# Kernel tuning notes

Measured on AMD Instinct MI355X. Metric: run time of the kernel, lower is better.

Reference implementation:

```python
import jax, jax.numpy as jnp
import numpy as np

B, S, H, D = 2, 2048, 16, 64


def setup_inputs() -> dict:
    key = jax.random.key(0)
    kq, kk, kv, km = jax.random.split(key, 4)
    q = jax.random.normal(kq, (B, S, H, D), dtype=jnp.float32)
    k = jax.random.normal(kk, (B, S, H, D), dtype=jnp.float32)
    v = jax.random.normal(kv, (B, S, H, D), dtype=jnp.float32)
    pattern_mask = jax.random.bernoulli(km, 0.1, (S, S))
    return {"q": q, "k": k, "v": v, "pattern_mask": pattern_mask}


def reference(q, k, v, pattern_mask):
    # Faithful math of the torch module: for each query row i, attend only to
    # columns j where pattern_mask[i, j]; softmax over the selected columns
    # per (batch, head); rows with no selected columns produce zeros.
    head_dim = q.shape[-1]
    scale = 1.0 / jnp.sqrt(jnp.asarray(head_dim, dtype=q.dtype))
    # scores: [B, H, S_q, S_k]
    scores = jnp.einsum('bihd,bjhd->bhij', q, k) * scale
    neg = jnp.finfo(scores.dtype).min
    masked = jnp.where(pattern_mask[None, None, :, :], scores, neg)
    attn = jax.nn.softmax(masked, axis=-1)
    # zero out rows with no active columns (softmax over all-masked row is uniform garbage)
    row_has = jnp.any(pattern_mask, axis=-1)  # [S]
    attn = jnp.where(row_has[None, None, :, None], attn, jnp.zeros((), dtype=attn.dtype))
    # output: [B, S, H, D]
    out = jnp.einsum('bhij,bjhd->bihd', attn, v)
    return out
```

## Files before the change

### kernel.cpp

```cpp
#include <hip/hip_runtime.h>
#include <hip/hip_bf16.h>
#include <math.h>

#define SLEN 2048
#define NBATCH 2
#define NH 16
#define DH 64
#define WPR 64
#define NROUND 32
#define TILEB 16384
#define CONVBLK (NBATCH * NH * NROUND)
#define PACKBLK (SLEN * WPR / 256)

typedef __attribute__((ext_vector_type(4))) short short4v;
typedef __attribute__((ext_vector_type(8))) short short8v;
typedef __attribute__((ext_vector_type(4))) float float4v;
typedef __attribute__((ext_vector_type(16))) float float16v;

__device__ __forceinline__ unsigned short f2bf(float f) {
  unsigned u = __float_as_uint(f);
  u += 0x7fffu + ((u >> 16) & 1u);
  return (unsigned short)(u >> 16);
}

__device__ __forceinline__ float fexp2(float x) {
#if __has_builtin(__builtin_amdgcn_exp2f)
  return __builtin_amdgcn_exp2f(x);
#else
  return __expf(x * 0.6931471805599453f);
#endif
}

__device__ __forceinline__ unsigned pack_bf2(float a, float b) {
  unsigned ua = __float_as_uint(a); ua += 0x7fffu + ((ua >> 16) & 1u);
  unsigned ub = __float_as_uint(b); ub += 0x7fffu + ((ub >> 16) & 1u);
  return __builtin_amdgcn_perm(ub, ua, 0x07060302u);
}

__device__ __forceinline__ unsigned cvtpk(float lo, float hi) {
  unsigned r;
  asm("v_cvt_pk_bf16_f32 %0, %1, %2" : "=v"(r) : "v"(lo), "v"(hi));
  return r;
}

__device__ __forceinline__ unsigned nib4(unsigned w) {
  return ((w * 0x01020408u) >> 24) & 0xFu;
}

__global__ __launch_bounds__(256) void prep_kernel(
    const float* __restrict__ kk, const float* __restrict__ vv,
    const void* __restrict__ mask,
    char* __restrict__ img, unsigned* __restrict__ packed) {
  const int tid = threadIdx.x;
  if (blockIdx.x >= CONVBLK) {
    const int w = (blockIdx.x - CONVBLK) * 256 + tid;
    const uint4* bp = (const uint4*)((const char*)mask + (size_t)w * 32);
    uint4 x = bp[0], y = bp[1];
    const unsigned orw = (x.x | x.y) | (x.z | x.w) | (y.x | y.y) | (y.z | y.w);
    __shared__ int s0, sm;
    if (tid == 0) { s0 = 0; sm = 0; }
    __syncthreads();
    const int lane0 = ((tid & 63) == 0);
    if (__any((orw & 0x000000ffu) != 0) && lane0) atomicOr(&s0, 1);
    if (__any((orw & 0xffffff00u) != 0) && lane0) atomicOr(&sm, 1);
    __syncthreads();
    unsigned bits;
    if (s0 && sm) {
      bits = nib4(x.x) | (nib4(x.y) << 4) | (nib4(x.z) << 8) | (nib4(x.w) << 12) |
             (nib4(y.x) << 16) | (nib4(y.y) << 20) | (nib4(y.z) << 24) | (nib4(y.w) << 28);
    } else {
      const unsigned* m = (const unsigned*)mask + (size_t)w * 32;
      bits = 0u;
#pragma unroll
      for (int j = 0; j < 32; j++) bits |= (m[j] ? 1u : 0u) << j;
    }
    packed[w] = bits;
    return;
  }
  const int bid = blockIdx.x;
  const int t = bid & 31;
  const int bh = bid >> 5;
  const int b = bh >> 4, h = bh & 15;
  char* timg = img + (size_t)bid * TILEB;

  {
    const int r = tid >> 2;
    const int dg = (tid & 3) << 4;
    const float* src = kk + (((size_t)(b * SLEN + t * 64 + r) * NH + h) * DH + dg);
    const int f = ((r >> 5) << 2) + (dg >> 4);
    char* base = timg + f * 1024 + (r & 31) * 16;
    float4v x0 = *(const float4v*)(src);
    float4v x1 = *(const float4v*)(src + 4);
    float4v x2 = *(const float4v*)(src + 8);
    float4v x3 = *(const float4v*)(src + 12);
    union { unsigned u[4]; short8v s8; } lo, hi;
    lo.u[0] = pack_bf2(x0.x, x0.y); lo.u[1] = pack_bf2(x0.z, x0.w);
    lo.u[2] = pack_bf2(x1.x, x1.y); lo.u[3] = pack_bf2(x1.z, x1.w);
    hi.u[0] = pack_bf2(x2.x, x2.y); hi.u[1] = pack_bf2(x2.z, x2.w);
    hi.u[2] = pack_bf2(x3.x, x3.y); hi.u[3] = pack_bf2(x3.z, x3.w);
    *(short8v*)(base) = lo.s8;
    *(short8v*)(base + 512) = hi.s8;
  }
  {
    const int d = tid >> 2;
    const int kg = (tid & 3) << 4;
    const float* src = vv + ((size_t)(b * SLEN + t * 64 + kg) * NH + h) * DH + d;
    const int fbase = 8 + ((d >> 5) << 2);
    const int l31d = d & 31;
#pragma unroll
    for (int i = 0; i < 16; i++) {
      const int p = kg + i;
      float x = src[(size_t)i * (NH * DH)];
      const int f = fbase + 2 * (p >> 5) + ((p >> 4) & 1);
      const int lane = ((p >> 2) & 1) * 32 + l31d;
      const int slot = 4 * ((p >> 3) & 1) + (p & 3);
      *(unsigned short*)(timg + f * 1024 + lane * 16 + slot * 2) = f2bf(x);
    }
  }
}

__global__ __launch_bounds__(256, 2) void sattn_fast8(
    const float* __restrict__ q, const unsigned* __restrict__ pmask,
    const char* __restrict__ img, float* __restrict__ out) {
  const int tid = threadIdx.x;
  const int xcd = blockIdx.x & 7;
  const int j = blockIdx.x >> 3;
  const int bh = xcd * 4 + (j >> 4);
  const int chunk = j & 15;
  const int b = bh >> 4;
  const int hd = bh & 15;
  const int wave = tid >> 6;
  const int lane = tid & 63;
  const int l31 = lane & 31;
  const int hl = lane >> 5;

  const int qrow = chunk * 128 + wave * 32 + l31;
  const int qw = qrow * WPR;

  const float SCL2 = 0.18033688011112042f;
  short8v qf[4];
  {
    const float* qp = q + (((size_t)b * SLEN + qrow) * NH + hd) * DH;
#pragma unroll
    for (int ds = 0; ds < 4; ds++) {
      float4v x0 = *(const float4v*)(qp + ds * 16 + hl * 8);
      float4v x1 = *(const float4v*)(qp + ds * 16 + hl * 8 + 4);
      union { unsigned u[4]; short8v s8; } cv;
      cv.u[0] = pack_bf2(x0.x * SCL2, x0.y * SCL2);
      cv.u[1] = pack_bf2(x0.z * SCL2, x0.w * SCL2);
      cv.u[2] = pack_bf2(x1.x * SCL2, x1.y * SCL2);
      cv.u[3] = pack_bf2(x1.z * SCL2, x1.w * SCL2);
      qf[ds] = cv.s8;
    }
  }

  const char* pt = img + (size_t)bh * (NROUND * TILEB) + lane * 16;

  float16v acc0 = {}, acc1 = {};
  float lsum = 0.f;

  short8v kf0 = *(const short8v*)(pt + 0 * 1024);
  short8v kf1 = *(const short8v*)(pt + 1 * 1024);
  short8v kf2 = *(const short8v*)(pt + 2 * 1024);
  short8v kf3 = *(const short8v*)(pt + 3 * 1024);
  short8v kf4 = *(const short8v*)(pt + 4 * 1024);
  short8v kf5 = *(const short8v*)(pt + 5 * 1024);
  short8v kf6 = *(const short8v*)(pt + 6 * 1024);
  short8v kf7 = *(const short8v*)(pt + 7 * 1024);
  short8v vf0 = *(const short8v*)(pt + 8 * 1024);
  short8v vf1 = *(const short8v*)(pt + 9 * 1024);
  short8v vf2 = *(const short8v*)(pt + 10 * 1024);
  short8v vf3 = *(const short8v*)(pt + 11 * 1024);
  short8v vf4 = *(const short8v*)(pt + 12 * 1024);
  short8v vf5 = *(const short8v*)(pt + 13 * 1024);
  short8v vf6 = *(const short8v*)(pt + 14 * 1024);
  short8v vf7 = *(const short8v*)(pt + 15 * 1024);
  uint2 m = *(const uint2*)&pmask[qw];

  for (int t = 0; t < NROUND; t++) {
    const unsigned m0 = m.x, m1 = m.y;
    const int tn = (t + 1 < NROUND) ? t + 1 : t;
    const char* pn = pt + (size_t)tn * TILEB;

    __builtin_amdgcn_s_setprio(1);
    float16v st0 = {}, st1 = {};
    st0 = __builtin_amdgcn_mfma_f32_32x32x16_bf16(kf0, qf[0], st0, 0, 0, 0);
    st1 = __builtin_amdgcn_mfma_f32_32x32x16_bf16(kf4, qf[0], st1, 0, 0, 0);
    st0 = __builtin_amdgcn_mfma_f32_32x32x16_bf16(kf1, qf[1], st0, 0, 0, 0);
    st1 = __builtin_amdgcn_mfma_f32_32x32x16_bf16(kf5, qf[1], st1, 0, 0, 0);
    st0 = __builtin_amdgcn_mfma_f32_32x32x16_bf16(kf2, qf[2], st0, 0, 0, 0);
    st1 = __builtin_amdgcn_mfma_f32_32x32x16_bf16(kf6, qf[2], st1, 0, 0, 0);
    st0 = __builtin_amdgcn_mfma_f32_32x32x16_bf16(kf3, qf[3], st0, 0, 0, 0);
    st1 = __builtin_amdgcn_mfma_f32_32x32x16_bf16(kf7, qf[3], st1, 0, 0, 0);
    __builtin_amdgcn_s_setprio(0);

    kf0 = *(const short8v*)(pn + 0 * 1024);
    kf1 = *(const short8v*)(pn + 1 * 1024);
    kf2 = *(const short8v*)(pn + 2 * 1024);
    kf3 = *(const short8v*)(pn + 3 * 1024);
    kf4 = *(const short8v*)(pn + 4 * 1024);
    kf5 = *(const short8v*)(pn + 5 * 1024);
    kf6 = *(const short8v*)(pn + 6 * 1024);
    kf7 = *(const short8v*)(pn + 7 * 1024);
    m = *(const uint2*)&pmask[qw + 2 * tn];

    float p0[16], p1[16];
#pragma unroll
    for (int u = 0; u < 4; u++) {
      const unsigned hw0 = m0 >> (8 * u + 4 * hl);
      const unsigned hw1 = m1 >> (8 * u + 4 * hl);
      {
        float a0 = fexp2(st0[4 * u + 0]); a0 = (hw0 & 1u) ? a0 : 0.f;
        float a1 = fexp2(st0[4 * u + 1]); a1 = (hw0 & 2u) ? a1 : 0.f;
        float a2 = fexp2(st0[4 * u + 2]); a2 = (hw0 & 4u) ? a2 : 0.f;
        float a3 = fexp2(st0[4 * u + 3]); a3 = (hw0 & 8u) ? a3 : 0.f;
        lsum += (a0 + a1) + (a2 + a3);
        p0[4 * u + 0] = a0; p0[4 * u + 1] = a1; p0[4 * u + 2] = a2; p0[4 * u + 3] = a3;
      }
      {
        float a0 = fexp2(st1[4 * u + 0]); a0 = (hw1 & 1u) ? a0 : 0.f;
        float a1 = fexp2(st1[4 * u + 1]); a1 = (hw1 & 2u) ? a1 : 0.f;
        float a2 = fexp2(st1[4 * u + 2]); a2 = (hw1 & 4u) ? a2 : 0.f;
        float a3 = fexp2(st1[4 * u + 3]); a3 = (hw1 & 8u) ? a3 : 0.f;
        lsum += (a0 + a1) + (a2 + a3);
        p1[4 * u + 0] = a0; p1[4 * u + 1] = a1; p1[4 * u + 2] = a2; p1[4 * u + 3] = a3;
      }
    }
    short8v pf0, pf1, pf2, pf3;
    {
      union { unsigned u[4]; short8v s8; } c0, c1, c2, c3;
#pragma unroll
      for (int jj = 0; jj < 4; jj++) {
        c0.u[jj] = cvtpk(p0[2 * jj], p0[2 * jj + 1]);
        c1.u[jj] = cvtpk(p0[8 + 2 * jj], p0[8 + 2 * jj + 1]);
        c2.u[jj] = cvtpk(p1[2 * jj], p1[2 * jj + 1]);
        c3.u[jj] = cvtpk(p1[8 + 2 * jj], p1[8 + 2 * jj + 1]);
      }
      pf0 = c0.s8; pf1 = c1.s8; pf2 = c2.s8; pf3 = c3.s8;
    }

    __builtin_amdgcn_s_setprio(1);
    acc0 = __builtin_amdgcn_mfma_f32_32x32x16_bf16(vf0, pf0, acc0, 0, 0, 0);
    acc1 = __builtin_amdgcn_mfma_f32_32x32x16_bf16(vf4, pf0, acc1, 0, 0, 0);
    acc0 = __builtin_amdgcn_mfma_f32_32x32x16_bf16(vf1, pf1, acc0, 0, 0, 0);
    acc1 = __builtin_amdgcn_mfma_f32_32x32x16_bf16(vf5, pf1, acc1, 0, 0, 0);
    acc0 = __builtin_amdgcn_mfma_f32_32x32x16_bf16(vf2, pf2, acc0, 0, 0, 0);
    acc1 = __builtin_amdgcn_mfma_f32_32x32x16_bf16(vf6, pf2, acc1, 0, 0, 0);
    acc0 = __builtin_amdgcn_mfma_f32_32x32x16_bf16(vf3, pf3, acc0, 0, 0, 0);
    acc1 = __builtin_amdgcn_mfma_f32_32x32x16_bf16(vf7, pf3, acc1, 0, 0, 0);
    __builtin_amdgcn_s_setprio(0);

    vf0 = *(const short8v*)(pn + 8 * 1024);
    vf1 = *(const short8v*)(pn + 9 * 1024);
    vf2 = *(const short8v*)(pn + 10 * 1024);
    vf3 = *(const short8v*)(pn + 11 * 1024);
    vf4 = *(const short8v*)(pn + 12 * 1024);
    vf5 = *(const short8v*)(pn + 13 * 1024);
    vf6 = *(const short8v*)(pn + 14 * 1024);
    vf7 = *(const short8v*)(pn + 15 * 1024);
  }

  lsum += __shfl_xor(lsum, 32);
  const float inv = (lsum > 0.f) ? 1.f / lsum : 0.f;
  float* op = out + (((size_t)b * SLEN + qrow) * NH + hd) * DH;
#pragma unroll
  for (int u = 0; u < 4; u++) {
    float4v o0, o1;
    o0.x = acc0[4 * u + 0] * inv; o0.y = acc0[4 * u + 1] * inv;
    o0.z = acc0[4 * u + 2] * inv; o0.w = acc0[4 * u + 3] * inv;
    o1.x = acc1[4 * u + 0] * inv; o1.y = acc1[4 * u + 1] * inv;
    o1.z = acc1[4 * u + 2] * inv; o1.w = acc1[4 * u + 3] * inv;
    *(float4v*)(op + 8 * u + 4 * hl) = o0;
    *(float4v*)(op + 32 + 8 * u + 4 * hl) = o1;
  }
}

__global__ __launch_bounds__(256) void sattn_fallback(
    const float* __restrict__ q, const float* __restrict__ kk,
    const float* __restrict__ vv, const unsigned int* __restrict__ pmask,
    float* __restrict__ out) {
  __shared__ __align__(16) unsigned short Kt[16 * 64];
  __shared__ __align__(16) unsigned short Vt[64 * 20];

  const int tid = threadIdx.x;
  const int chunk = blockIdx.x & 31;
  const int bh = blockIdx.x >> 5;
  const int b = bh >> 4;
  const int h = bh & 15;
  const int wave = tid >> 6;
  const int lane = tid & 63;
  const int lq = lane & 15;
  const int g = lane >> 4;

  const int qrow = chunk * 64 + wave * 16 + lq;

  short4v qf[4];
  {
    const float* qp = q + (((size_t)b * SLEN + qrow) * NH + h) * DH;
#pragma unroll
    for (int ks = 0; ks < 4; ks++) {
      float4v x = *(const float4v*)(qp + ks * 16 + g * 4);
      short4v s;
      s.x = (short)f2bf(x.x); s.y = (short)f2bf(x.y);
      s.z = (short)f2bf(x.z); s.w = (short)f2bf(x.w);
      qf[ks] = s;
    }
  }

  const int srow = tid >> 4;
  const int scol = (tid & 15) * 4;
  const size_t kvbase = (size_t)b * SLEN * (NH * DH) + (size_t)h * DH;

  float4v acc[4] = {};
  float m_run = -INFINITY;
  float l_run = 0.f;

  for (int t = 0; t < SLEN / 16; t++) {
    const int kbase = t * 16;
    __syncthreads();
    {
      const size_t rowoff = kvbase + (size_t)(kbase + srow) * (NH * DH) + scol;
      float4v x = *(const float4v*)(kk + rowoff);
      short4v s;
      s.x = (short)f2bf(x.x); s.y = (short)f2bf(x.y);
      s.z = (short)f2bf(x.z); s.w = (short)f2bf(x.w);
      const int off = (scol * 2) ^ ((srow & 7) << 4);
      *(short4v*)((char*)Kt + srow * 128 + off) = s;

      float4v y = *(const float4v*)(vv + rowoff);
      Vt[(scol + 0) * 20 + srow] = f2bf(y.x);
      Vt[(scol + 1) * 20 + srow] = f2bf(y.y);
      Vt[(scol + 2) * 20 + srow] = f2bf(y.z);
      Vt[(scol + 3) * 20 + srow] = f2bf(y.w);
    }
    __syncthreads();

    float4v stv = {0.f, 0.f, 0.f, 0.f};
#pragma unroll
    for (int ks = 0; ks < 4; ks++) {
      const int off = ((ks * 16 + g * 4) * 2) ^ ((lq & 7) << 4);
      short4v kf = *(const short4v*)((const char*)Kt + lq * 128 + off);
      stv = __builtin_amdgcn_mfma_f32_16x16x16bf16_1k(kf, qf[ks], stv, 0, 0, 0);
    }

    const unsigned int mw = pmask[qrow * WPR + (kbase >> 5)];
    const int shift = (kbase & 16) + g * 4;
    float sc[4];
    float tmax = -INFINITY;
#pragma unroll
    for (int r = 0; r < 4; r++) {
      bool a = (mw >> (shift + r)) & 1u;
      sc[r] = a ? stv[r] * 0.125f : -INFINITY;
      tmax = fmaxf(tmax, sc[r]);
    }
    tmax = fmaxf(tmax, __shfl_xor(tmax, 16));
    tmax = fmaxf(tmax, __shfl_xor(tmax, 32));
    const float mnew = fmaxf(m_run, tmax);
    const float muse = (mnew > -1e37f) ? mnew : 0.f;
    const float alpha = __expf(m_run - muse);
    float p[4], tsum = 0.f;
#pragma unroll
    for (int r = 0; r < 4; r++) {
      p[r] = __expf(sc[r] - muse);
      tsum += p[r];
    }
    tsum += __shfl_xor(tsum, 16);
    tsum += __shfl_xor(tsum, 32);
    l_run = l_run * alpha + tsum;
    m_run = mnew;

    short4v pfv;
    pfv.x = (short)f2bf(p[0]); pfv.y = (short)f2bf(p[1]);
    pfv.z = (short)f2bf(p[2]); pfv.w = (short)f2bf(p[3]);

#pragma unroll
    for (int n = 0; n < 4; n++) {
      acc[n][0] *= alpha; acc[n][1] *= alpha;
      acc[n][2] *= alpha; acc[n][3] *= alpha;
      short4v vf = *(const short4v*)((const char*)Vt + ((n * 16 + lq) * 20 + g * 4) * 2);
      acc[n] = __builtin_amdgcn_mfma_f32_16x16x16bf16_1k(vf, pfv, acc[n], 0, 0, 0);
    }
  }

  const float inv = (l_run > 0.f) ? 1.f / l_run : 0.f;
  float* op = out + (((size_t)b * SLEN + qrow) * NH + h) * DH;
#pragma unroll
  for (int n = 0; n < 4; n++) {
    float4v o;
    o.x = acc[n][0] * inv; o.y = acc[n][1] * inv;
    o.z = acc[n][2] * inv; o.w = acc[n][3] * inv;
    *(float4v*)(op + n * 16 + g * 4) = o;
  }
}

extern "C" void kernel_launch(void* const* d_in, const int* in_sizes, int n_in,
                              void* d_out, int out_size, void* d_ws, size_t ws_size,
                              hipStream_t stream) {
  const float* q = (const float*)d_in[0];
  const float* k = (const float*)d_in[1];
  const float* v = (const float*)d_in[2];
  const void* mask = d_in[3];
  float* out = (float*)d_out;

  unsigned int* packed = (unsigned int*)((char*)d_ws + 256);
  char* img = (char*)d_ws + (1 << 20);
  const size_t need = (size_t)(1 << 20) + (size_t)CONVBLK * TILEB;

  prep_kernel<<<CONVBLK + PACKBLK, 256, 0, stream>>>(k, v, mask, img, packed);
  if (ws_size >= need) {
    sattn_fast8<<<NBATCH * NH * (SLEN / 128), 256, 0, stream>>>(q, packed, img, out);
  } else {
    sattn_fallback<<<NBATCH * NH * (SLEN / 64), 256, 0, stream>>>(q, k, v, packed, out);
  }
}
```

Before: 69.59 us.

## Split key range across wave pairs with LDS reduction to double block count

Each block now covers 64 query rows instead of 128. The four waves form two pairs, and each pair processes half of the 32 key tiles. The partial accumulators and row sums from the second half are combined through shared memory before the final normalization and store. The grid doubles and the launch bound allows 4 blocks per CU, which raises parallelism and shortens each wave's serial loop, at the cost of a shared-memory reduction, a block barrier, and more register pressure under the tighter occupancy target.

```diff
diff --git a/kernel.cpp b/kernel.cpp
--- a/kernel.cpp
+++ b/kernel.cpp
@@ -119,23 +119,27 @@
   }
 }
 
-__global__ __launch_bounds__(256, 2) void sattn_fast8(
+__global__ __launch_bounds__(256, 4) void sattn_fast9(
     const float* __restrict__ q, const unsigned* __restrict__ pmask,
     const char* __restrict__ img, float* __restrict__ out) {
+  __shared__ float red[2][64][33];
+
   const int tid = threadIdx.x;
   const int xcd = blockIdx.x & 7;
   const int j = blockIdx.x >> 3;
-  const int bh = xcd * 4 + (j >> 4);
-  const int chunk = j & 15;
+  const int bh = xcd * 4 + (j >> 5);
+  const int chunk = j & 31;
   const int b = bh >> 4;
   const int hd = bh & 15;
   const int wave = tid >> 6;
   const int lane = tid & 63;
   const int l31 = lane & 31;
   const int hl = lane >> 5;
-
-  const int qrow = chunk * 128 + wave * 32 + l31;
-  const int qw = qrow * WPR;
+  const int qsub = wave & 1;
+  const int khalf = wave >> 1;
+
+  const int qrow = chunk * 64 + qsub * 32 + l31;
+  const int qw = qrow * WPR + 2 * (khalf * 16);
 
   const float SCL2 = 0.18033688011112042f;
   short8v qf[4];
@@ -154,7 +158,7 @@
     }
   }
 
-  const char* pt = img + (size_t)bh * (NROUND * TILEB) + lane * 16;
+  const char* pt = img + ((size_t)bh * NROUND + khalf * 16) * TILEB + lane * 16;
 
   float16v acc0 = {}, acc1 = {};
   float lsum = 0.f;
@@ -177,9 +181,9 @@
   short8v vf7 = *(const short8v*)(pt + 15 * 1024);
   uint2 m = *(const uint2*)&pmask[qw];
 
-  for (int t = 0; t < NROUND; t++) {
+  for (int t = 0; t < 16; t++) {
     const unsigned m0 = m.x, m1 = m.y;
-    const int tn = (t + 1 < NROUND) ? t + 1 : t;
+    const int tn = (t + 1 < 16) ? t + 1 : t;
     const char* pn = pt + (size_t)tn * TILEB;
 
     __builtin_amdgcn_s_setprio(1);
@@ -261,17 +265,36 @@
   }
 
   lsum += __shfl_xor(lsum, 32);
-  const float inv = (lsum > 0.f) ? 1.f / lsum : 0.f;
-  float* op = out + (((size_t)b * SLEN + qrow) * NH + hd) * DH;
-#pragma unroll
-  for (int u = 0; u < 4; u++) {
-    float4v o0, o1;
-    o0.x = acc0[4 * u + 0] * inv; o0.y = acc0[4 * u + 1] * inv;
-    o0.z = acc0[4 * u + 2] * inv; o0.w = acc0[4 * u + 3] * inv;
-    o1.x = acc1[4 * u + 0] * inv; o1.y = acc1[4 * u + 1] * inv;
-    o1.z = acc1[4 * u + 2] * inv; o1.w = acc1[4 * u + 3] * inv;
-    *(float4v*)(op + 8 * u + 4 * hl) = o0;
-    *(float4v*)(op + 32 + 8 * u + 4 * hl) = o1;
+
+  if (khalf == 1) {
+    float* rp = &red[qsub][lane][0];
+#pragma unroll
+    for (int u = 0; u < 16; u++) {
+      rp[u] = acc0[u];
+      rp[16 + u] = acc1[u];
+    }
+    rp[32] = lsum;
+  }
+  __syncthreads();
+  if (khalf == 0) {
+    const float* rp = &red[qsub][lane][0];
+    const float l = lsum + rp[32];
+    const float inv = (l > 0.f) ? 1.f / l : 0.f;
+    float* op = out + (((size_t)b * SLEN + qrow) * NH + hd) * DH;
+#pragma unroll
+    for (int u = 0; u < 4; u++) {
+      float4v o0, o1;
+      o0.x = (acc0[4 * u + 0] + rp[4 * u + 0]) * inv;
+      o0.y = (acc0[4 * u + 1] + rp[4 * u + 1]) * inv;
+      o0.z = (acc0[4 * u + 2] + rp[4 * u + 2]) * inv;
+      o0.w = (acc0[4 * u + 3] + rp[4 * u + 3]) * inv;
+      o1.x = (acc1[4 * u + 0] + rp[16 + 4 * u + 0]) * inv;
+      o1.y = (acc1[4 * u + 1] + rp[16 + 4 * u + 1]) * inv;
+      o1.z = (acc1[4 * u + 2] + rp[16 + 4 * u + 2]) * inv;
+      o1.w = (acc1[4 * u + 3] + rp[16 + 4 * u + 3]) * inv;
+      *(float4v*)(op + 8 * u + 4 * hl) = o0;
+      *(float4v*)(op + 32 + 8 * u + 4 * hl) = o1;
+    }
   }
 }
 
@@ -408,7 +431,7 @@
 
   prep_kernel<<<CONVBLK + PACKBLK, 256, 0, stream>>>(k, v, mask, img, packed);
   if (ws_size >= need) {
-    sattn_fast8<<<NBATCH * NH * (SLEN / 128), 256, 0, stream>>>(q, packed, img, out);
+    sattn_fast9<<<NBATCH * NH * (SLEN / 64), 256, 0, stream>>>(q, packed, img, out);
   } else {
     sattn_fallback<<<NBATCH * NH * (SLEN / 64), 256, 0, stream>>>(q, k, v, packed, out);
   }
```

Measured after the change: 203.0 us. 2.92x slower.
